# Performance work log

Measured on AMD Instinct MI355X. Metric: run time of the kernel, lower is better.

## Reference

```python
import jax, jax.numpy as jnp
import numpy as np

B, C, H, W = 4, 64, 64, 64
INTER = max(1, C // 8)


def setup_inputs() -> dict:
    key = jax.random.key(0)
    ks = jax.random.split(key, 8)
    return {
        "x": jax.random.normal(ks[0], (B, C, H, W), dtype=jnp.float32),
        "Wq": jax.random.normal(ks[1], (INTER, C), dtype=jnp.float32) * 0.1,
        "bq": jax.random.normal(ks[2], (INTER,), dtype=jnp.float32) * 0.1,
        "Wk": jax.random.normal(ks[3], (INTER, C), dtype=jnp.float32) * 0.1,
        "bk": jax.random.normal(ks[4], (INTER,), dtype=jnp.float32) * 0.1,
        "Wv": jax.random.normal(ks[5], (C, C), dtype=jnp.float32) * 0.1,
        "bv": jax.random.normal(ks[6], (C,), dtype=jnp.float32) * 0.1,
        "gamma": jax.random.normal(ks[7], (1,), dtype=jnp.float32),
    }


def reference(x, Wq, bq, Wk, bk, Wv, bv, gamma):
    b, c, h, w = x.shape
    n = h * w
    xf = x.reshape(b, c, n)  # flatten spatial dims, [B, C, N]
    # 1x1 convs == per-pixel matmuls
    q = jnp.einsum('ic,bcn->bin', Wq, xf) + bq[None, :, None]  # [B, inter, N]
    k = jnp.einsum('ic,bcn->bin', Wk, xf) + bk[None, :, None]  # [B, inter, N]
    v = jnp.einsum('oc,bcn->bon', Wv, xf) + bv[None, :, None]  # [B, C, N]
    # energy[b,n,m] = sum_i q[b,i,n] * k[b,i,m]  (unscaled attention)
    energy = jnp.einsum('bin,bim->bnm', q, k)  # [B, N, N]
    attn = jax.nn.softmax(energy, axis=-1)
    # out[b,c,n] = sum_m v[b,c,m] * attn[b,n,m]
    out = jnp.einsum('bcm,bnm->bcn', v, attn).reshape(b, c, h, w)
    return gamma[0] * out + x
```

## Files before the change

### kernel.cpp

```cpp
#include <hip/hip_runtime.h>
#include <hip/hip_bf16.h>


#define NPIX 4096
#define LOG2E 1.44269504088896f
typedef __attribute__((ext_vector_type(8))) short s8v;
typedef __attribute__((ext_vector_type(4))) float f4v;

static __device__ __forceinline__ unsigned short f2bf(float f) {
    union { float f; unsigned u; } v; v.f = f;
    unsigned r = v.u + 0x7FFFu + ((v.u >> 16) & 1u);
    return (unsigned short)(r >> 16);
}
static __device__ __forceinline__ unsigned pkbf2(float a, float b) {
    __hip_bfloat162 h = __float22bfloat162_rn(make_float2(a, b));
    return *reinterpret_cast<unsigned*>(&h);
}
static __device__ __forceinline__ float fexp2(float x) {
#if __has_builtin(__builtin_amdgcn_exp2f)
    return __builtin_amdgcn_exp2f(x);
#else
    return exp2f(x);
#endif
}

extern "C" __global__ void __launch_bounds__(256, 4) qkv_kernel(
    const float* __restrict__ x,
    const float* __restrict__ Wq, const float* __restrict__ bq,
    const float* __restrict__ Wk, const float* __restrict__ bk,
    const float* __restrict__ Wv, const float* __restrict__ bv,
    unsigned short* __restrict__ qt, unsigned short* __restrict__ kt,
    unsigned short* __restrict__ vb)
{
    __shared__ float xs[64][17];
    __shared__ __align__(16) float wls[80][68];
    __shared__ float bls[80];
    const int t = threadIdx.x;
    const int b = blockIdx.x >> 8, n0 = (blockIdx.x & 255) << 4;

    for (int e = t; e < 1024; e += 256) {
        int c = e >> 4, j = e & 15;
        xs[c][j] = x[((b << 6) + c) * NPIX + n0 + j];
    }
    for (int e = t; e < 5120; e += 256) {
        int row = e >> 6, cc = e & 63;
        float wv = (e < 512) ? Wq[e] * LOG2E : (e < 1024) ? Wk[e - 512] : Wv[e - 1024];
        wls[row][cc] = wv;
    }
    if (t < 80) bls[t] = (t < 8) ? bq[t] * LOG2E : (t < 16) ? bk[t - 8] : bv[t - 16];
    __syncthreads();

    const int j = t & 15, oh = t >> 4;
    float xr[64];
#pragma unroll
    for (int c = 0; c < 64; ++c) xr[c] = xs[c][j];

    const int n = n0 + j;
#pragma unroll
    for (int r = 0; r < 5; ++r) {
        const int row = oh * 5 + r;
        float acc = bls[row];
#pragma unroll
        for (int q = 0; q < 16; ++q) {
            float4 wv = *(const float4*)&wls[row][q * 4];
            acc += wv.x * xr[4*q] + wv.y * xr[4*q+1] + wv.z * xr[4*q+2] + wv.w * xr[4*q+3];
        }
        const unsigned short h = f2bf(acc);
        if (row < 8)       qt[(b * NPIX + n) * 8 + row] = h;
        else if (row < 16) kt[(b * NPIX + n) * 8 + row - 8] = h;
        else               vb[((b << 6) + (row - 16)) * NPIX + n] = h;
    }
}

extern "C" __global__ void __launch_bounds__(512, 4) attn_kernel(
    const unsigned short* __restrict__ qt, const unsigned short* __restrict__ kt,
    const unsigned short* __restrict__ vb,
    const float* __restrict__ x, const float* __restrict__ gamma_p,
    float* __restrict__ out)
{
    __shared__ __align__(16) unsigned short vls[4][64][64];
    __shared__ __align__(16) unsigned short pls[8][16][72];
    __shared__ float Lred[4][2][16];

    const int t = threadIdx.x;
    const int w = t >> 6, lane = t & 63, g = lane >> 4, c16 = lane & 15;
    const int gg = w >> 1, wg = w & 1;
    const int bid = ((blockIdx.x & 7) << 6) + (blockIdx.x >> 3);
    const int b = bid >> 7, n0 = (bid & 127) << 5;

    const unsigned short* qtB = qt + b * NPIX * 8;
    const unsigned short* ktB = kt + b * NPIX * 8;
    const unsigned short* vbB = vb + (b << 6) * NPIX;

    s8v qfr = {0,0,0,0,0,0,0,0};
    if (g == 0) qfr = *(const s8v*)(qtB + (n0 + wg * 16 + c16) * 8);

    const int t2 = t & 127;
    const int vc = t2 >> 1, hh = t2 & 1;
    const int mbase = gg << 10;

    f4v accO[4];
#pragma unroll
    for (int cs = 0; cs < 4; ++cs) { accO[cs][0]=0.f; accO[cs][1]=0.f; accO[cs][2]=0.f; accO[cs][3]=0.f; }
    float lsum = 0.f;

    s8v vr[4], kf[4];
    {
        const unsigned short* vp = vbB + vc * NPIX + mbase + hh * 32;
        vr[0] = *(const s8v*)(vp);      vr[1] = *(const s8v*)(vp + 8);
        vr[2] = *(const s8v*)(vp + 16); vr[3] = *(const s8v*)(vp + 24);
#pragma unroll
        for (int ms = 0; ms < 4; ++ms) {
            s8v z = {0,0,0,0,0,0,0,0};
            kf[ms] = z;
            if (g == 0) kf[ms] = *(const s8v*)(ktB + (mbase + ms * 16 + c16) * 8);
        }
    }

    for (int ti = 0; ti < 16; ++ti) {
#pragma unroll
        for (int q = 0; q < 4; ++q) {
            const int pos = (hh * 4 + q) ^ (vc & 7);
            *(s8v*)&vls[gg][vc][pos * 8] = vr[q];
        }
        __syncthreads();

        const int m1 = mbase + ((ti + 1) << 6);
        if (ti < 15) {
            const unsigned short* vp = vbB + vc * NPIX + m1 + hh * 32;
            vr[0] = *(const s8v*)(vp);      vr[1] = *(const s8v*)(vp + 8);
            vr[2] = *(const s8v*)(vp + 16); vr[3] = *(const s8v*)(vp + 24);
        }

        f4v sm[4];
#pragma unroll
        for (int ms = 0; ms < 4; ++ms) {
            f4v z; z[0]=0.f; z[1]=0.f; z[2]=0.f; z[3]=0.f;
            sm[ms] = __builtin_amdgcn_mfma_f32_16x16x32_bf16(kf[ms], qfr, z, 0, 0, 0);
        }
        if (ti < 15) {
#pragma unroll
            for (int ms = 0; ms < 4; ++ms)
                if (g == 0) kf[ms] = *(const s8v*)(ktB + (m1 + ms * 16 + c16) * 8);
        }

#pragma unroll
        for (int ms = 0; ms < 4; ++ms) {
            float p0 = fexp2(sm[ms][0]), p1 = fexp2(sm[ms][1]);
            float p2 = fexp2(sm[ms][2]), p3 = fexp2(sm[ms][3]);
            lsum += (p0 + p1) + (p2 + p3);
            uint2 pk; pk.x = pkbf2(p0, p1); pk.y = pkbf2(p2, p3);
            *(uint2*)&pls[w][c16][ms * 16 + g * 4] = pk;
        }
        __builtin_amdgcn_wave_barrier();

        s8v pf0 = *(const s8v*)&pls[w][c16][g * 8];
        s8v pf1 = *(const s8v*)&pls[w][c16][32 + g * 8];

#pragma unroll
        for (int cs = 0; cs < 4; ++cs) {
            const int c = cs * 16 + c16;
            const int q0 = (g)     ^ (c16 & 7);
            const int q1 = (4 + g) ^ (c16 & 7);
            s8v vf0 = *(const s8v*)&vls[gg][c][q0 * 8];
            s8v vf1 = *(const s8v*)&vls[gg][c][q1 * 8];
            accO[cs] = __builtin_amdgcn_mfma_f32_16x16x32_bf16(vf0, pf0, accO[cs], 0, 0, 0);
            accO[cs] = __builtin_amdgcn_mfma_f32_16x16x32_bf16(vf1, pf1, accO[cs], 0, 0, 0);
        }
        __syncthreads();
    }

    lsum += __shfl_xor(lsum, 16);
    lsum += __shfl_xor(lsum, 32);
    if (g == 0) Lred[gg][wg][c16] = lsum;

    float (*ored)[128][17] = reinterpret_cast<float(*)[128][17]>(&vls[0][0][0]);
    const int s2 = t & 127;
    if (gg >= 2) {
#pragma unroll
        for (int cs = 0; cs < 4; ++cs)
#pragma unroll
            for (int r = 0; r < 4; ++r) ored[gg - 2][s2][cs * 4 + r] = accO[cs][r];
    }
    __syncthreads();
    if (gg < 2) {
#pragma unroll
        for (int cs = 0; cs < 4; ++cs)
#pragma unroll
            for (int r = 0; r < 4; ++r) accO[cs][r] += ored[gg][s2][cs * 4 + r];
    }
    __syncthreads();
    if (gg == 1) {
#pragma unroll
        for (int cs = 0; cs < 4; ++cs)
#pragma unroll
            for (int r = 0; r < 4; ++r) ored[0][s2][cs * 4 + r] = accO[cs][r];
    }
    __syncthreads();
    if (gg == 0) {
#pragma unroll
        for (int cs = 0; cs < 4; ++cs)
#pragma unroll
            for (int r = 0; r < 4; ++r) accO[cs][r] += ored[0][s2][cs * 4 + r];

        const float L = Lred[0][wg][c16] + Lred[1][wg][c16]
                      + Lred[2][wg][c16] + Lred[3][wg][c16];
        const float inv = 1.0f / L;
        const float gm = gamma_p[0];
        const int n = n0 + wg * 16 + c16;
#pragma unroll
        for (int cs = 0; cs < 4; ++cs)
#pragma unroll
            for (int r = 0; r < 4; ++r) {
                const int c = cs * 16 + g * 4 + r;
                const int gi = ((b << 6) + c) * NPIX + n;
                out[gi] = gm * (accO[cs][r] * inv) + x[gi];
            }
    }
}

extern "C" void kernel_launch(void* const* d_in, const int* in_sizes, int n_in,
                              void* d_out, int out_size, void* d_ws, size_t ws_size,
                              hipStream_t stream) {
    const float* x     = (const float*)d_in[0];
    const float* Wq    = (const float*)d_in[1];
    const float* bq    = (const float*)d_in[2];
    const float* Wk    = (const float*)d_in[3];
    const float* bk    = (const float*)d_in[4];
    const float* Wv    = (const float*)d_in[5];
    const float* bv    = (const float*)d_in[6];
    const float* gamma = (const float*)d_in[7];

    unsigned short* qt = (unsigned short*)d_ws;
    unsigned short* kt = qt + 4 * NPIX * 8;
    unsigned short* vb = kt + 4 * NPIX * 8;

    qkv_kernel<<<1024, 256, 0, stream>>>(x, Wq, bq, Wk, bk, Wv, bv, qt, kt, vb);
    attn_kernel<<<512, 512, 0, stream>>>(qt, kt, vb, x, gamma, (float*)d_out);
}
```

Before: 112.0 us.

## Double-buffer V tile in LDS and keep P in registers via 16x16x16 MFMA

Switches the QK^T and PV products from 16x16x32 bf16 MFMA to 16x16x16 MFMA. For QK^T this uses half-width fragments so lanes in groups 0-1 each carry 4 of the 8 inter channels instead of padding with zeros. The MFMA output layout for P then matches the B-operand layout directly, so the per-wave LDS round trip for P and its wave barrier are removed. The V tile in LDS is double-buffered so the next tile is written after compute, cutting the block barriers per iteration from two to one. The costs are twice as many MFMA instructions for PV, more LDS use from the second V buffer (which may lower occupancy), and narrower LDS reads.

Result: no change. 111.7 us (-0.3%).

```diff
diff --git a/kernel.cpp b/kernel.cpp
--- a/kernel.cpp
+++ b/kernel.cpp
@@ -5,6 +5,7 @@
 #define NPIX 4096
 #define LOG2E 1.44269504088896f
 typedef __attribute__((ext_vector_type(8))) short s8v;
+typedef __attribute__((ext_vector_type(4))) short s4v;
 typedef __attribute__((ext_vector_type(4))) float f4v;
 
 static __device__ __forceinline__ unsigned short f2bf(float f) {
@@ -21,6 +22,16 @@
     return __builtin_amdgcn_exp2f(x);
 #else
     return exp2f(x);
+#endif
+}
+
+static __device__ __forceinline__ f4v mfma16(s4v a, s4v b, f4v c) {
+#if __has_builtin(__builtin_amdgcn_mfma_f32_16x16x16bf16_1k)
+    return __builtin_amdgcn_mfma_f32_16x16x16bf16_1k(a, b, c, 0, 0, 0);
+#else
+    s8v a8 = {a[0], a[1], a[2], a[3], 0, 0, 0, 0};
+    s8v b8 = {b[0], b[1], b[2], b[3], 0, 0, 0, 0};
+    return __builtin_amdgcn_mfma_f32_16x16x32_bf16(a8, b8, c, 0, 0, 0);
 #endif
 }
 
@@ -78,8 +89,7 @@
     const float* __restrict__ x, const float* __restrict__ gamma_p,
     float* __restrict__ out)
 {
-    __shared__ __align__(16) unsigned short vls[4][64][64];
-    __shared__ __align__(16) unsigned short pls[8][16][72];
+    __shared__ __align__(16) unsigned short vls[2][4][64][64];
     __shared__ float Lred[4][2][16];
 
     const int t = threadIdx.x;
@@ -92,8 +102,8 @@
     const unsigned short* ktB = kt + b * NPIX * 8;
     const unsigned short* vbB = vb + (b << 6) * NPIX;
 
-    s8v qfr = {0,0,0,0,0,0,0,0};
-    if (g == 0) qfr = *(const s8v*)(qtB + (n0 + wg * 16 + c16) * 8);
+    s4v qfr = {0, 0, 0, 0};
+    if (g < 2) qfr = *(const s4v*)(qtB + (n0 + wg * 16 + c16) * 8 + g * 4);
 
     const int t2 = t & 127;
     const int vc = t2 >> 1, hh = t2 & 1;
@@ -104,77 +114,88 @@
     for (int cs = 0; cs < 4; ++cs) { accO[cs][0]=0.f; accO[cs][1]=0.f; accO[cs][2]=0.f; accO[cs][3]=0.f; }
     float lsum = 0.f;
 
-    s8v vr[4], kf[4];
+    s8v vr[4];
+    s4v kf[4], kfn[4];
     {
         const unsigned short* vp = vbB + vc * NPIX + mbase + hh * 32;
         vr[0] = *(const s8v*)(vp);      vr[1] = *(const s8v*)(vp + 8);
         vr[2] = *(const s8v*)(vp + 16); vr[3] = *(const s8v*)(vp + 24);
 #pragma unroll
         for (int ms = 0; ms < 4; ++ms) {
-            s8v z = {0,0,0,0,0,0,0,0};
+            s4v z = {0, 0, 0, 0};
             kf[ms] = z;
-            if (g == 0) kf[ms] = *(const s8v*)(ktB + (mbase + ms * 16 + c16) * 8);
-        }
-    }
-
-    for (int ti = 0; ti < 16; ++ti) {
+            if (g < 2) kf[ms] = *(const s4v*)(ktB + (mbase + ms * 16 + c16) * 8 + g * 4);
+        }
 #pragma unroll
         for (int q = 0; q < 4; ++q) {
             const int pos = (hh * 4 + q) ^ (vc & 7);
-            *(s8v*)&vls[gg][vc][pos * 8] = vr[q];
-        }
-        __syncthreads();
-
+            *(s8v*)&vls[0][gg][vc][pos * 8] = vr[q];
+        }
+    }
+    __syncthreads();
+
+    int cur = 0;
+    for (int ti = 0; ti < 16; ++ti) {
         const int m1 = mbase + ((ti + 1) << 6);
         if (ti < 15) {
             const unsigned short* vp = vbB + vc * NPIX + m1 + hh * 32;
             vr[0] = *(const s8v*)(vp);      vr[1] = *(const s8v*)(vp + 8);
             vr[2] = *(const s8v*)(vp + 16); vr[3] = *(const s8v*)(vp + 24);
+#pragma unroll
+            for (int ms = 0; ms < 4; ++ms) {
+                s4v z = {0, 0, 0, 0};
+                kfn[ms] = z;
+                if (g < 2) kfn[ms] = *(const s4v*)(ktB + (m1 + ms * 16 + c16) * 8 + g * 4);
+            }
         }
 
         f4v sm[4];
 #pragma unroll
         for (int ms = 0; ms < 4; ++ms) {
             f4v z; z[0]=0.f; z[1]=0.f; z[2]=0.f; z[3]=0.f;
-            sm[ms] = __builtin_amdgcn_mfma_f32_16x16x32_bf16(kf[ms], qfr, z, 0, 0, 0);
-        }
-        if (ti < 15) {
-#pragma unroll
-            for (int ms = 0; ms < 4; ++ms)
-                if (g == 0) kf[ms] = *(const s8v*)(ktB + (m1 + ms * 16 + c16) * 8);
-        }
-
+            sm[ms] = mfma16(kf[ms], qfr, z);
+        }
+
+        s4v pf[4];
 #pragma unroll
         for (int ms = 0; ms < 4; ++ms) {
             float p0 = fexp2(sm[ms][0]), p1 = fexp2(sm[ms][1]);
             float p2 = fexp2(sm[ms][2]), p3 = fexp2(sm[ms][3]);
             lsum += (p0 + p1) + (p2 + p3);
-            uint2 pk; pk.x = pkbf2(p0, p1); pk.y = pkbf2(p2, p3);
-            *(uint2*)&pls[w][c16][ms * 16 + g * 4] = pk;
-        }
-        __builtin_amdgcn_wave_barrier();
-
-        s8v pf0 = *(const s8v*)&pls[w][c16][g * 8];
-        s8v pf1 = *(const s8v*)&pls[w][c16][32 + g * 8];
+            union { uint2 u; s4v v; } pu;
+            pu.u.x = pkbf2(p0, p1); pu.u.y = pkbf2(p2, p3);
+            pf[ms] = pu.v;
+        }
 
 #pragma unroll
         for (int cs = 0; cs < 4; ++cs) {
             const int c = cs * 16 + c16;
-            const int q0 = (g)     ^ (c16 & 7);
-            const int q1 = (4 + g) ^ (c16 & 7);
-            s8v vf0 = *(const s8v*)&vls[gg][c][q0 * 8];
-            s8v vf1 = *(const s8v*)&vls[gg][c][q1 * 8];
-            accO[cs] = __builtin_amdgcn_mfma_f32_16x16x32_bf16(vf0, pf0, accO[cs], 0, 0, 0);
-            accO[cs] = __builtin_amdgcn_mfma_f32_16x16x32_bf16(vf1, pf1, accO[cs], 0, 0, 0);
+#pragma unroll
+            for (int ms = 0; ms < 4; ++ms) {
+                const int pos = (2 * ms + (g >> 1)) ^ (c & 7);
+                s4v vf = *(const s4v*)&vls[cur][gg][c][pos * 8 + (g & 1) * 4];
+                accO[cs] = mfma16(vf, pf[ms], accO[cs]);
+            }
+        }
+
+        if (ti < 15) {
+#pragma unroll
+            for (int q = 0; q < 4; ++q) {
+                const int pos = (hh * 4 + q) ^ (vc & 7);
+                *(s8v*)&vls[cur ^ 1][gg][vc][pos * 8] = vr[q];
+            }
+#pragma unroll
+            for (int ms = 0; ms < 4; ++ms) kf[ms] = kfn[ms];
         }
         __syncthreads();
+        cur ^= 1;
     }
 
     lsum += __shfl_xor(lsum, 16);
     lsum += __shfl_xor(lsum, 32);
     if (g == 0) Lred[gg][wg][c16] = lsum;
 
-    float (*ored)[128][17] = reinterpret_cast<float(*)[128][17]>(&vls[0][0][0]);
+    float (*ored)[128][17] = reinterpret_cast<float(*)[128][17]>(&vls[0][0][0][0]);
     const int s2 = t & 127;
     if (gg >= 2) {
 #pragma unroll
```
